# Kernel optimization log

Measured on AMD Instinct MI355X. Metric: run time of the kernel, lower is better.

## Reference

```python
import jax, jax.numpy as jnp
import numpy as np

EPS = 10.0
MAX_ITER = 50
THRESH = 1e-05
N, M, D = 8192, 8192, 32


def setup_inputs() -> dict:
    key = jax.random.key(0)
    k1, k2, k3, k4 = jax.random.split(key, 4)
    x = jax.random.normal(k1, (N, D), dtype=jnp.float32)
    y = jax.random.normal(k2, (M, D), dtype=jnp.float32)
    p = jax.random.uniform(k3, (N,), dtype=jnp.float32)
    q = jax.random.uniform(k4, (M,), dtype=jnp.float32)
    p = p / jnp.sum(p)  # marginals must be probability vectors
    q = q / jnp.sum(q)
    return {"x": x, "y": y, "p": p, "q": q}


def _cost_matrix_l2(x, y):
    # ||x_i - y_j||^2 via the expansion, avoiding the [N, M, D] intermediate
    x2 = jnp.sum(x * x, axis=-1)  # [N]
    y2 = jnp.sum(y * y, axis=-1)  # [M]
    C = x2[:, None] + y2[None, :] - 2.0 * (x @ y.T)  # [N, M]
    return jnp.maximum(C, 0.0)


def reference(x, y, p, q):
    C = _cost_matrix_l2(x, y)          # [N, M]
    K = jnp.exp(-C / EPS)              # [N, M]

    def step(carry, _):
        a, b, done = carry
        a_new = p / (K @ b)            # [N]
        b_new = q / (K.T @ a_new)      # [M]
        err = jnp.linalg.norm(b_new - b)
        # emulate the early break: freeze (a, b) once err < thresh was hit
        a_out = jnp.where(done, a, a_new)
        b_out = jnp.where(done, b, b_new)
        done = jnp.logical_or(done, err < THRESH)
        return (a_out, b_out, done), None

    init = (jnp.zeros_like(p), jnp.ones_like(q), jnp.array(False))
    (a, b, _), _ = jax.lax.scan(step, init, None, length=MAX_ITER)

    T = a[:, None] * K * b[None, :]    # diag(a) @ K @ diag(b)
    w_cost = jnp.sum(T * C)
    return w_cost, T
```

## Files before the change

kernel.cpp:

```cpp
#include <hip/hip_runtime.h>
#include <hip/hip_fp16.h>


#define NN 8192
#define DDIM 32
#define EPSF 10.0f
#define LOG2E 1.44269504088896340736f
#define LN2F 0.69314718055994530942f
#define KLOG2 8.0f
#define THRESH2 1e-10f

#define OFF_KS   0ull
#define OFF_PART (67108864ull)
#define OFF_A    (OFF_PART + 8388608ull)
#define OFF_B    (OFF_A + 32768ull)
#define OFF_X2   (OFF_B + 32768ull)
#define OFF_Y2   (OFF_X2 + 32768ull)
#define OFF_ERR  (OFF_Y2 + 32768ull)
#define WS_NEEDED (OFF_ERR + 4096ull)

typedef float floatx2 __attribute__((ext_vector_type(2)));

#if __has_builtin(__builtin_amdgcn_cvt_pk_f32_fp8) && __has_builtin(__builtin_amdgcn_cvt_pk_fp8_f32)
#define HW_FP8 1
#else
#define HW_FP8 0
#include <hip/hip_fp8.h>
#endif

__device__ __forceinline__ void fp8x4_to_f32(unsigned int w, float* f) {
#if HW_FP8
    floatx2 lo = __builtin_amdgcn_cvt_pk_f32_fp8((int)w, false);
    floatx2 hi = __builtin_amdgcn_cvt_pk_f32_fp8((int)w, true);
    f[0] = lo.x; f[1] = lo.y; f[2] = hi.x; f[3] = hi.y;
#else
    for (int i = 0; i < 4; ++i) {
        __hip_fp8_e4m3 h; h.__x = (__hip_fp8_storage_t)((w >> (8 * i)) & 0xff);
        f[i] = (float)h;
    }
#endif
}

__device__ __forceinline__ unsigned char f32_to_fp8(float v) {
#if HW_FP8
    return (unsigned char)(__builtin_amdgcn_cvt_pk_fp8_f32(v, v, 0, false) & 0xff);
#else
    __hip_fp8_e4m3 h(v);
    return (unsigned char)h.__x;
#endif
}

__device__ __forceinline__ bool is_done(const float* __restrict__ errpart) {
    float e = 0.f;
    for (int k = 0; k < 256; ++k) e += errpart[k];
    return e < THRESH2;
}

__global__ __launch_bounds__(256) void k_init(const float* __restrict__ x,
                                              const float* __restrict__ y,
                                              float* __restrict__ x2,
                                              float* __restrict__ y2,
                                              float* __restrict__ b,
                                              float* __restrict__ errpart,
                                              float* __restrict__ out) {
    int t = blockIdx.x * 256 + threadIdx.x;
    const float4* x4 = (const float4*)(x + (size_t)t * DDIM);
    float s = 0.f;
#pragma unroll
    for (int k = 0; k < 8; ++k) { float4 v = x4[k]; s += v.x*v.x + v.y*v.y + v.z*v.z + v.w*v.w; }
    x2[t] = s;
    const float4* y4 = (const float4*)(y + (size_t)t * DDIM);
    s = 0.f;
#pragma unroll
    for (int k = 0; k < 8; ++k) { float4 v = y4[k]; s += v.x*v.x + v.y*v.y + v.z*v.z + v.w*v.w; }
    y2[t] = s;
    b[t] = 1.0f;
    if (t < 256) errpart[t] = 1e30f;
    if (t == 0) out[0] = 0.f;
}

__global__ __launch_bounds__(256) void k_build(const float* __restrict__ x,
                                               const float* __restrict__ y,
                                               const float* __restrict__ x2,
                                               const float* __restrict__ y2,
                                               unsigned char* __restrict__ Ks) {
    __shared__ float yT[DDIM][256];
    __shared__ float xT[DDIM][32];
    __shared__ __align__(16) unsigned char hb8[32][256];
    const int t = threadIdx.x;
    const int jb = blockIdx.x & 31;
    const int ib = blockIdx.x >> 5;
    const int colbase = jb * 256, rowbase = ib * 32;

    {
        const float4* yp = (const float4*)(y + (size_t)(colbase + t) * DDIM);
#pragma unroll
        for (int k = 0; k < 8; ++k) {
            float4 v = yp[k];
            yT[4*k+0][t] = v.x; yT[4*k+1][t] = v.y; yT[4*k+2][t] = v.z; yT[4*k+3][t] = v.w;
        }
    }
    {
        int r = t >> 3, ds = (t & 7) * 4;
        float4 v = *(const float4*)(x + (size_t)(rowbase + r) * DDIM + ds);
        xT[ds+0][r] = v.x; xT[ds+1][r] = v.y; xT[ds+2][r] = v.z; xT[ds+3][r] = v.w;
    }
    __syncthreads();

    float acc[32];
#pragma unroll
    for (int r = 0; r < 32; ++r) acc[r] = 0.f;
    for (int d = 0; d < DDIM; ++d) {
        float yv = yT[d][t];
#pragma unroll
        for (int r4 = 0; r4 < 8; ++r4) {
            float4 xv = *(const float4*)&xT[d][r4 * 4];
            acc[r4*4+0] = fmaf(xv.x, yv, acc[r4*4+0]);
            acc[r4*4+1] = fmaf(xv.y, yv, acc[r4*4+1]);
            acc[r4*4+2] = fmaf(xv.z, yv, acc[r4*4+2]);
            acc[r4*4+3] = fmaf(xv.w, yv, acc[r4*4+3]);
        }
    }
    const float y2c = y2[colbase + t];
#pragma unroll
    for (int r = 0; r < 32; ++r) {
        float Cv = fmaxf(x2[rowbase + r] + y2c - 2.f * acc[r], 0.f);
        float arg = KLOG2 - Cv * (LOG2E / EPSF);
        hb8[r][t] = f32_to_fp8(__builtin_amdgcn_exp2f(arg));
    }
    __syncthreads();
    {
        int row = t >> 3, off = (t & 7) * 32;
        uint4 v0 = *(const uint4*)&hb8[row][off];
        uint4 v1 = *(const uint4*)&hb8[row][off + 16];
        unsigned char* dst = Ks + (size_t)(rowbase + row) * NN + colbase + off;
        *(uint4*)dst = v0;
        *(uint4*)(dst + 16) = v1;
    }
}

__global__ __launch_bounds__(1024) void k_iter(const unsigned char* __restrict__ Ks,
                                               const float* __restrict__ bg,
                                               const float* __restrict__ p,
                                               float* __restrict__ a_out,
                                               float* __restrict__ part,
                                               const float* __restrict__ errpart) {
    if (is_done(errpart)) return;
    __shared__ float bsw[NN];
    __shared__ float arow[32];
    __shared__ float rowhalf[8][2];
    const int t = threadIdx.x;
    const int w = t >> 6, lane = t & 63;
    const int band = blockIdx.x * 32;

    {
        float4 g0 = ((const float4*)bg)[2 * t];
        float4 g1 = ((const float4*)bg)[2 * t + 1];
        float vals[8] = {g0.x, g0.y, g0.z, g0.w, g1.x, g1.y, g1.z, g1.w};
        int c0 = t * 8;
#pragma unroll
        for (int u = 0; u < 8; ++u) {
            int c = c0 + u;
            bsw[(c >> 10) * 1024 + ((c >> 2) & 3) * 256 + ((c >> 4) & 63) * 4 + (c & 3)] = vals[u];
        }
    }
    __syncthreads();

    float cacc[8] = {0.f, 0.f, 0.f, 0.f, 0.f, 0.f, 0.f, 0.f};
    const float4* b4 = (const float4*)bsw;

    for (int sub = 0; sub < 4; ++sub) {
        const int rl = w >> 1, half = w & 1;
        const int rglob = band + sub * 8 + rl;
        const uint4* kp = (const uint4*)(Ks + (size_t)rglob * NN + half * 4096);
        float rs = 0.f;
#pragma unroll
        for (int c = 0; c < 4; ++c) {
            uint4 kv = kp[c * 64 + lane];
            const unsigned int* kw = (const unsigned int*)&kv;
            const int kc = half * 4 + c;
#pragma unroll
            for (int j4 = 0; j4 < 4; ++j4) {
                float kf[4];
                fp8x4_to_f32(kw[j4], kf);
                float4 bv = b4[(kc * 4 + j4) * 64 + lane];
                rs = fmaf(kf[0], bv.x, rs);
                rs = fmaf(kf[1], bv.y, rs);
                rs = fmaf(kf[2], bv.z, rs);
                rs = fmaf(kf[3], bv.w, rs);
            }
        }
#pragma unroll
        for (int off = 32; off > 0; off >>= 1) rs += __shfl_down(rs, off, 64);
        if (lane == 0) rowhalf[rl][half] = rs;
        __syncthreads();
        if (t < 8) {
            int rg = band + sub * 8 + t;
            float av = p[rg] / (rowhalf[t][0] + rowhalf[t][1]);
            arow[sub * 8 + t] = av;
            a_out[rg] = av;
        }
        __syncthreads();
        const uint2* kp2 = (const uint2*)(Ks + (size_t)(band + sub * 8) * NN);
#pragma unroll
        for (int r8 = 0; r8 < 8; ++r8) {
            uint2 kv = kp2[r8 * (NN / 8) + t];
            float kf[8];
            fp8x4_to_f32(kv.x, kf);
            fp8x4_to_f32(kv.y, kf + 4);
            float av = arow[sub * 8 + r8];
#pragma unroll
            for (int j = 0; j < 8; ++j) cacc[j] = fmaf(kf[j], av, cacc[j]);
        }
    }
    float4* pp = (float4*)(part + (size_t)blockIdx.x * NN + t * 8);
    pp[0] = make_float4(cacc[0], cacc[1], cacc[2], cacc[3]);
    pp[1] = make_float4(cacc[4], cacc[5], cacc[6], cacc[7]);
}

__global__ __launch_bounds__(256) void k_div(const float* __restrict__ part,
                                             const float* __restrict__ q,
                                             float* __restrict__ b,
                                             float* __restrict__ errpart) {
    if (is_done(errpart)) return;
    const int t = threadIdx.x;
    const int c = t & 31, ibc = t >> 5;
    const int col = blockIdx.x * 32 + c;
    float s = 0.f;
#pragma unroll 4
    for (int i = 0; i < 32; ++i) s += part[(size_t)(ibc * 32 + i) * NN + col];
    __shared__ float red[8][32];
    __shared__ float esc[32];
    red[ibc][c] = s;
    __syncthreads();
    if (ibc == 0) {
        float sum = 0.f;
#pragma unroll
        for (int k = 0; k < 8; ++k) sum += red[k][c];
        float bn = q[col] / sum;
        float d = bn - b[col];
        b[col] = bn;
        esc[c] = d * d;
    }
    __syncthreads();
    if (t == 0) {
        float e = 0.f;
#pragma unroll
        for (int k = 0; k < 32; ++k) e += esc[k];
        errpart[blockIdx.x] = e;
    }
}

__global__ __launch_bounds__(256) void k_final(const unsigned char* __restrict__ Ks,
                                               const float* __restrict__ a,
                                               const float* __restrict__ b,
                                               float* __restrict__ out) {
    const int t = threadIdx.x;
    const int row = blockIdx.x;
    const float ai = a[row];
    const uint2* kp = (const uint2*)(Ks + (size_t)row * NN);
    float* Trow = out + 1 + (size_t)row * NN;
    float w = 0.f;
    const float c1 = EPSF * LN2F;
#pragma unroll
    for (int k = 0; k < 4; ++k) {
        const int col = k * 2048 + t * 8;
        uint2 kv = kp[k * 256 + t];
        float kf[8];
        fp8x4_to_f32(kv.x, kf);
        fp8x4_to_f32(kv.y, kf + 4);
        float4 b0 = *(const float4*)(b + col);
        float4 b1 = *(const float4*)(b + col + 4);
        float bv[8] = {b0.x, b0.y, b0.z, b0.w, b1.x, b1.y, b1.z, b1.w};
#pragma unroll
        for (int j = 0; j < 8; ++j) {
            float ks = kf[j];
            float Tv = ai * ks * bv[j];
            float Cv = c1 * (KLOG2 - __builtin_amdgcn_logf(fmaxf(ks, 1e-35f)));
            w = fmaf(Tv, Cv, w);
            Trow[col + j] = Tv;
        }
    }
#pragma unroll
    for (int off = 32; off > 0; off >>= 1) w += __shfl_down(w, off, 64);
    __shared__ float red[4];
    if ((t & 63) == 0) red[t >> 6] = w;
    __syncthreads();
    if (t == 0) atomicAdd(out, (red[0] + red[1]) + (red[2] + red[3]));
}

extern "C" void kernel_launch(void* const* d_in, const int* in_sizes, int n_in,
                              void* d_out, int out_size, void* d_ws, size_t ws_size,
                              hipStream_t stream) {
    const float* x = (const float*)d_in[0];
    const float* y = (const float*)d_in[1];
    const float* p = (const float*)d_in[2];
    const float* q = (const float*)d_in[3];
    float* out = (float*)d_out;
    if (ws_size < WS_NEEDED) return;
    char* ws = (char*)d_ws;
    unsigned char* Ks = (unsigned char*)(ws + OFF_KS);
    float* part = (float*)(ws + OFF_PART);
    float* a = (float*)(ws + OFF_A);
    float* b = (float*)(ws + OFF_B);
    float* x2 = (float*)(ws + OFF_X2);
    float* y2 = (float*)(ws + OFF_Y2);
    float* errpart = (float*)(ws + OFF_ERR);

    k_init<<<dim3(32), dim3(256), 0, stream>>>(x, y, x2, y2, b, errpart, out);
    k_build<<<dim3(8192), dim3(256), 0, stream>>>(x, y, x2, y2, Ks);
    for (int it = 0; it < 50; ++it) {
        k_iter<<<dim3(256), dim3(1024), 0, stream>>>(Ks, b, p, a, part, errpart);
        k_div<<<dim3(256), dim3(256), 0, stream>>>(part, q, b, errpart);
    }
    k_final<<<dim3(8192), dim3(256), 0, stream>>>(Ks, a, b, out);
}
```

Baseline: 2.076 ms.

## Prefetch next K rows and parallelize convergence check in Sinkhorn iteration kernels

```diff
diff --git a/kernel.cpp b/kernel.cpp
--- a/kernel.cpp
+++ b/kernel.cpp
@@ -48,12 +48,6 @@
     __hip_fp8_e4m3 h(v);
     return (unsigned char)h.__x;
 #endif
-}
-
-__device__ __forceinline__ bool is_done(const float* __restrict__ errpart) {
-    float e = 0.f;
-    for (int k = 0; k < 256; ++k) e += errpart[k];
-    return e < THRESH2;
 }
 
 __global__ __launch_bounds__(256) void k_init(const float* __restrict__ x,
@@ -139,23 +133,56 @@
     }
 }
 
+#define ROWFMA(KV, KC) { \
+    const unsigned int* kw_ = (const unsigned int*)&(KV); \
+    _Pragma("unroll") \
+    for (int j4 = 0; j4 < 4; ++j4) { \
+        float kf_[4]; \
+        fp8x4_to_f32(kw_[j4], kf_); \
+        float4 bv_ = b4[((KC) * 4 + j4) * 64 + lane]; \
+        rs = fmaf(kf_[0], bv_.x, rs); \
+        rs = fmaf(kf_[1], bv_.y, rs); \
+        rs = fmaf(kf_[2], bv_.z, rs); \
+        rs = fmaf(kf_[3], bv_.w, rs); \
+    } }
+
+#define COLFMA(KV, AV) { \
+    float kf_[8]; \
+    fp8x4_to_f32((KV).x, kf_); \
+    fp8x4_to_f32((KV).y, kf_ + 4); \
+    _Pragma("unroll") \
+    for (int j = 0; j < 8; ++j) cacc[j] = fmaf(kf_[j], (AV), cacc[j]); }
+
 __global__ __launch_bounds__(1024) void k_iter(const unsigned char* __restrict__ Ks,
                                                const float* __restrict__ bg,
                                                const float* __restrict__ p,
                                                float* __restrict__ a_out,
                                                float* __restrict__ part,
                                                const float* __restrict__ errpart) {
-    if (is_done(errpart)) return;
     __shared__ float bsw[NN];
-    __shared__ float arow[32];
-    __shared__ float rowhalf[8][2];
+    __shared__ float rowhalf[2][8][2];
+    __shared__ float dred[17];
     const int t = threadIdx.x;
     const int w = t >> 6, lane = t & 63;
     const int band = blockIdx.x * 32;
-
-    {
-        float4 g0 = ((const float4*)bg)[2 * t];
-        float4 g1 = ((const float4*)bg)[2 * t + 1];
+    const int rl = w >> 1, half = w & 1;
+
+    float4 g0 = ((const float4*)bg)[2 * t];
+    float4 g1 = ((const float4*)bg)[2 * t + 1];
+    float e = (t < 256) ? errpart[t] : 0.f;
+    const uint4* kp0 = (const uint4*)(Ks + (size_t)(band + rl) * NN + half * 4096);
+    uint4 ka0 = kp0[lane], ka1 = kp0[64 + lane], ka2 = kp0[128 + lane], ka3 = kp0[192 + lane];
+    __builtin_amdgcn_sched_barrier(0);
+
+#pragma unroll
+    for (int off = 32; off > 0; off >>= 1) e += __shfl_down(e, off, 64);
+    if (lane == 0) dred[w] = e;
+    __syncthreads();
+    if (t == 0) dred[16] = (dred[0] + dred[1]) + (dred[2] + dred[3]);
+    __syncthreads();
+    if (dred[16] < THRESH2) return;
+
+    {
         float vals[8] = {g0.x, g0.y, g0.z, g0.w, g1.x, g1.y, g1.z, g1.w};
         int c0 = t * 8;
 #pragma unroll
@@ -169,49 +196,55 @@
     float cacc[8] = {0.f, 0.f, 0.f, 0.f, 0.f, 0.f, 0.f, 0.f};
     const float4* b4 = (const float4*)bsw;
 
+#pragma unroll
     for (int sub = 0; sub < 4; ++sub) {
-        const int rl = w >> 1, half = w & 1;
-        const int rglob = band + sub * 8 + rl;
-        const uint4* kp = (const uint4*)(Ks + (size_t)rglob * NN + half * 4096);
+        const int sb = sub & 1;
+        const uint2* kp2 = (const uint2*)(Ks + (size_t)(band + sub * 8) * NN);
+        uint2 cv0 = kp2[0 * (NN / 8) + t], cv1 = kp2[1 * (NN / 8) + t],
+              cv2 = kp2[2 * (NN / 8) + t], cv3 = kp2[3 * (NN / 8) + t],
+              cv4 = kp2[4 * (NN / 8) + t], cv5 = kp2[5 * (NN / 8) + t],
+              cv6 = kp2[6 * (NN / 8) + t], cv7 = kp2[7 * (NN / 8) + t];
+        uint4 kb0 = {0,0,0,0}, kb1 = {0,0,0,0}, kb2 = {0,0,0,0}, kb3 = {0,0,0,0};
+        if (sub < 3) {
+            const uint4* kp = (const uint4*)(Ks + (size_t)(band + (sub + 1) * 8 + rl) * NN + half * 4096);
+            kb0 = kp[lane]; kb1 = kp[64 + lane]; kb2 = kp[128 + lane]; kb3 = kp[192 + lane];
+        }
+        __builtin_amdgcn_sched_barrier(0);
+
         float rs = 0.f;
-#pragma unroll
-        for (int c = 0; c < 4; ++c) {
-            uint4 kv = kp[c * 64 + lane];
-            const unsigned int* kw = (const unsigned int*)&kv;
-            const int kc = half * 4 + c;
-#pragma unroll
-            for (int j4 = 0; j4 < 4; ++j4) {
-                float kf[4];
-                fp8x4_to_f32(kw[j4], kf);
-                float4 bv = b4[(kc * 4 + j4) * 64 + lane];
-                rs = fmaf(kf[0], bv.x, rs);
-                rs = fmaf(kf[1], bv.y, rs);
-                rs = fmaf(kf[2], bv.z, rs);
-                rs = fmaf(kf[3], bv.w, rs);
-            }
-        }
+        ROWFMA(ka0, half * 4 + 0)
+        ROWFMA(ka1, half * 4 + 1)
+        ROWFMA(ka2, half * 4 + 2)
+        ROWFMA(ka3, half * 4 + 3)
 #pragma unroll
         for (int off = 32; off > 0; off >>= 1) rs += __shfl_down(rs, off, 64);
-        if (lane == 0) rowhalf[rl][half] = rs;
+        if (lane == 0) rowhalf[sb][rl][half] = rs;
         __syncthreads();
-        if (t < 8) {
-            int rg = band + sub * 8 + t;
-            float av = p[rg] / (rowhalf[t][0] + rowhalf[t][1]);
-            arow[sub * 8 + t] = av;
-            a_out[rg] = av;
-        }
-        __syncthreads();
-        const uint2* kp2 = (const uint2*)(Ks + (size_t)(band + sub * 8) * NN);
-#pragma unroll
-        for (int r8 = 0; r8 < 8; ++r8) {
-            uint2 kv = kp2[r8 * (NN / 8) + t];
-            float kf[8];
-            fp8x4_to_f32(kv.x, kf);
-            fp8x4_to_f32(kv.y, kf + 4);
-            float av = arow[sub * 8 + r8];
-#pragma unroll
-            for (int j = 0; j < 8; ++j) cacc[j] = fmaf(kf[j], av, cacc[j]);
-        }
+
+        const int rg = band + sub * 8;
+        float av0 = p[rg + 0] / (rowhalf[sb][0][0] + rowhalf[sb][0][1]);
+        float av1 = p[rg + 1] / (rowhalf[sb][1][0] + rowhalf[sb][1][1]);
+        float av2 = p[rg + 2] / (rowhalf[sb][2][0] + rowhalf[sb][2][1]);
+        float av3 = p[rg + 3] / (rowhalf[sb][3][0] + rowhalf[sb][3][1]);
+        float av4 = p[rg + 4] / (rowhalf[sb][4][0] + rowhalf[sb][4][1]);
+        float av5 = p[rg + 5] / (rowhalf[sb][5][0] + rowhalf[sb][5][1]);
+        float av6 = p[rg + 6] / (rowhalf[sb][6][0] + rowhalf[sb][6][1]);
+        float av7 = p[rg + 7] / (rowhalf[sb][7][0] + rowhalf[sb][7][1]);
+        if (t == 0) {
+            *(float4*)(a_out + rg)     = make_float4(av0, av1, av2, av3);
+            *(float4*)(a_out + rg + 4) = make_float4(av4, av5, av6, av7);
+        }
+
+        COLFMA(cv0, av0)
+        COLFMA(cv1, av1)
+        COLFMA(cv2, av2)
+        COLFMA(cv3, av3)
+        COLFMA(cv4, av4)
+        COLFMA(cv5, av5)
+        COLFMA(cv6, av6)
+        COLFMA(cv7, av7)
+
+        if (sub < 3) { ka0 = kb0; ka1 = kb1; ka2 = kb2; ka3 = kb3; }
     }
     float4* pp = (float4*)(part + (size_t)blockIdx.x * NN + t * 8);
     pp[0] = make_float4(cacc[0], cacc[1], cacc[2], cacc[3]);
@@ -222,15 +255,25 @@
                                              const float* __restrict__ q,
                                              float* __restrict__ b,
                                              float* __restrict__ errpart) {
-    if (is_done(errpart)) return;
     const int t = threadIdx.x;
+    __shared__ float red[8][32];
+    __shared__ float esc[32];
+    __shared__ float dsum[5];
+    {
+        float e = errpart[t];
+#pragma unroll
+        for (int off = 32; off > 0; off >>= 1) e += __shfl_down(e, off, 64);
+        if ((t & 63) == 0) dsum[t >> 6] = e;
+        __syncthreads();
+        if (t == 0) dsum[4] = (dsum[0] + dsum[1]) + (dsum[2] + dsum[3]);
+        __syncthreads();
+        if (dsum[4] < THRESH2) return;
+    }
     const int c = t & 31, ibc = t >> 5;
     const int col = blockIdx.x * 32 + c;
     float s = 0.f;
 #pragma unroll 4
     for (int i = 0; i < 32; ++i) s += part[(size_t)(ibc * 32 + i) * NN + col];
-    __shared__ float red[8][32];
-    __shared__ float esc[32];
     red[ibc][c] = s;
     __syncthreads();
     if (ibc == 0) {
```

New measurement: 1.755 ms. 15.5% less time.

## Load K band once into registers and reuse for row and column products

Applied to the files above, without the earlier changes.

```diff
diff --git a/kernel.cpp b/kernel.cpp
--- a/kernel.cpp
+++ b/kernel.cpp
@@ -50,18 +50,12 @@
 #endif
 }
 
-__device__ __forceinline__ bool is_done(const float* __restrict__ errpart) {
-    float e = 0.f;
-    for (int k = 0; k < 256; ++k) e += errpart[k];
-    return e < THRESH2;
-}
-
 __global__ __launch_bounds__(256) void k_init(const float* __restrict__ x,
                                               const float* __restrict__ y,
                                               float* __restrict__ x2,
                                               float* __restrict__ y2,
                                               float* __restrict__ b,
-                                              float* __restrict__ errpart,
+                                              float* __restrict__ err,
                                               float* __restrict__ out) {
     int t = blockIdx.x * 256 + threadIdx.x;
     const float4* x4 = (const float4*)(x + (size_t)t * DDIM);
@@ -75,7 +69,7 @@
     for (int k = 0; k < 8; ++k) { float4 v = y4[k]; s += v.x*v.x + v.y*v.y + v.z*v.z + v.w*v.w; }
     y2[t] = s;
     b[t] = 1.0f;
-    if (t < 256) errpart[t] = 1e30f;
+    if (t < 2) err[t] = 1e30f;
     if (t == 0) out[0] = 0.f;
 }
 
@@ -139,79 +133,117 @@
     }
 }
 
+__device__ __forceinline__ float rowdot8(uint2 kv, const float4 b0, const float4 b1) {
+    float kf[8];
+    fp8x4_to_f32(kv.x, kf);
+    fp8x4_to_f32(kv.y, kf + 4);
+    float r = kf[0] * b0.x;
+    r = fmaf(kf[1], b0.y, r); r = fmaf(kf[2], b0.z, r); r = fmaf(kf[3], b0.w, r);
+    r = fmaf(kf[4], b1.x, r); r = fmaf(kf[5], b1.y, r);
+    r = fmaf(kf[6], b1.z, r); r = fmaf(kf[7], b1.w, r);
+    return r;
+}
+
+__device__ __forceinline__ void colfma8(uint2 kv, float av, float* cacc) {
+    float kf[8];
+    fp8x4_to_f32(kv.x, kf);
+    fp8x4_to_f32(kv.y, kf + 4);
+#pragma unroll
+    for (int j = 0; j < 8; ++j) cacc[j] = fmaf(kf[j], av, cacc[j]);
+}
+
+__device__ __forceinline__ float wave_reduce_rows8(float s0, float s1, float s2, float s3,
+                                                   float s4, float s5, float s6, float s7,
+                                                   int lane) {
+    const bool q0 = lane & 1, q1 = lane & 2, q2 = lane & 4;
+    float e0 = q0 ? s1 : s0, o0 = q0 ? s0 : s1;
+    float e1 = q0 ? s3 : s2, o1 = q0 ? s2 : s3;
+    float e2 = q0 ? s5 : s4, o2 = q0 ? s4 : s5;
+    float e3 = q0 ? s7 : s6, o3 = q0 ? s6 : s7;
+    e0 += __shfl_xor(o0, 1, 64);
+    e1 += __shfl_xor(o1, 1, 64);
+    e2 += __shfl_xor(o2, 1, 64);
+    e3 += __shfl_xor(o3, 1, 64);
+    float f0 = q1 ? e1 : e0, g0 = q1 ? e0 : e1;
+    float f1 = q1 ? e3 : e2, g1 = q1 ? e2 : e3;
+    f0 += __shfl_xor(g0, 2, 64);
+    f1 += __shfl_xor(g1, 2, 64);
+    float h = q2 ? f1 : f0, i8 = q2 ? f0 : f1;
+    h += __shfl_xor(i8, 4, 64);
+    h += __shfl_xor(h, 8, 64);
+    h += __shfl_xor(h, 16, 64);
+    h += __shfl_xor(h, 32, 64);
+    return h;
+}
+
 __global__ __launch_bounds__(1024) void k_iter(const unsigned char* __restrict__ Ks,
                                                const float* __restrict__ bg,
                                                const float* __restrict__ p,
                                                float* __restrict__ a_out,
                                                float* __restrict__ part,
-                                               const float* __restrict__ errpart) {
-    if (is_done(errpart)) return;
-    __shared__ float bsw[NN];
-    __shared__ float arow[32];
-    __shared__ float rowhalf[8][2];
+                                               float* __restrict__ err, int it) {
     const int t = threadIdx.x;
+    if (blockIdx.x == 0 && t == 0) err[it & 1] = 0.f;
+    if (err[(it ^ 1) & 1] < THRESH2) return;
+
     const int w = t >> 6, lane = t & 63;
-    const int band = blockIdx.x * 32;
-
-    {
-        float4 g0 = ((const float4*)bg)[2 * t];
-        float4 g1 = ((const float4*)bg)[2 * t + 1];
-        float vals[8] = {g0.x, g0.y, g0.z, g0.w, g1.x, g1.y, g1.z, g1.w};
-        int c0 = t * 8;
-#pragma unroll
-        for (int u = 0; u < 8; ++u) {
-            int c = c0 + u;
-            bsw[(c >> 10) * 1024 + ((c >> 2) & 3) * 256 + ((c >> 4) & 63) * 4 + (c & 3)] = vals[u];
-        }
-    }
-    __syncthreads();
+    const int band = blockIdx.x << 5;
+
+    const float4 bv0 = ((const float4*)bg)[2 * t];
+    const float4 bv1 = ((const float4*)bg)[2 * t + 1];
+    float pv = 0.f;
+    if (w == 0 && lane < 32) pv = p[band + lane];
+
+    __shared__ float wred[2][16][8];
+    __shared__ float a8s[2][8];
+
+    const uint2* kp = (const uint2*)(Ks + (size_t)band * NN) + t;
+    uint2 c0 = kp[0 * 1024], c1 = kp[1 * 1024], c2 = kp[2 * 1024], c3 = kp[3 * 1024],
+          c4 = kp[4 * 1024], c5 = kp[5 * 1024], c6 = kp[6 * 1024], c7 = kp[7 * 1024];
 
     float cacc[8] = {0.f, 0.f, 0.f, 0.f, 0.f, 0.f, 0.f, 0.f};
-    const float4* b4 = (const float4*)bsw;
-
+
+#pragma unroll
     for (int sub = 0; sub < 4; ++sub) {
-        const int rl = w >> 1, half = w & 1;
-        const int rglob = band + sub * 8 + rl;
-        const uint4* kp = (const uint4*)(Ks + (size_t)rglob * NN + half * 4096);
-        float rs = 0.f;
-#pragma unroll
-        for (int c = 0; c < 4; ++c) {
-            uint4 kv = kp[c * 64 + lane];
-            const unsigned int* kw = (const unsigned int*)&kv;
-            const int kc = half * 4 + c;
-#pragma unroll
-            for (int j4 = 0; j4 < 4; ++j4) {
-                float kf[4];
-                fp8x4_to_f32(kw[j4], kf);
-                float4 bv = b4[(kc * 4 + j4) * 64 + lane];
-                rs = fmaf(kf[0], bv.x, rs);
-                rs = fmaf(kf[1], bv.y, rs);
-                rs = fmaf(kf[2], bv.z, rs);
-                rs = fmaf(kf[3], bv.w, rs);
+        const int sb = sub & 1;
+        uint2 n0 = c0, n1 = c1, n2 = c2, n3 = c3, n4 = c4, n5 = c5, n6 = c6, n7 = c7;
+        if (sub < 3) {
+            const uint2* kn = kp + (size_t)(sub + 1) * 8 * 1024;
+            n0 = kn[0 * 1024]; n1 = kn[1 * 1024]; n2 = kn[2 * 1024]; n3 = kn[3 * 1024];
+            n4 = kn[4 * 1024]; n5 = kn[5 * 1024]; n6 = kn[6 * 1024]; n7 = kn[7 * 1024];
+        }
+        __builtin_amdgcn_sched_barrier(0);
+
+        float s0 = rowdot8(c0, bv0, bv1), s1 = rowdot8(c1, bv0, bv1);
+        float s2 = rowdot8(c2, bv0, bv1), s3 = rowdot8(c3, bv0, bv1);
+        float s4 = rowdot8(c4, bv0, bv1), s5 = rowdot8(c5, bv0, bv1);
+        float s6 = rowdot8(c6, bv0, bv1), s7 = rowdot8(c7, bv0, bv1);
+        float h = wave_reduce_rows8(s0, s1, s2, s3, s4, s5, s6, s7, lane);
+        if (lane < 8) wred[sb][w][lane] = h;
+        __syncthreads();
+
+        if (w == 0) {
+            float v = wred[sb][lane >> 3][lane & 7] + wred[sb][8 + (lane >> 3)][lane & 7];
+            v += __shfl_xor(v, 8, 64);
+            v += __shfl_xor(v, 16, 64);
+            v += __shfl_xor(v, 32, 64);
+            float pw = __shfl(pv, sub * 8 + (lane & 7), 64);
+            if (lane < 8) {
+                float av = pw / v;
+                a8s[sb][lane] = av;
+                a_out[band + sub * 8 + lane] = av;
             }
         }
-#pragma unroll
-        for (int off = 32; off > 0; off >>= 1) rs += __shfl_down(rs, off, 64);
-        if (lane == 0) rowhalf[rl][half] = rs;
         __syncthreads();
-        if (t < 8) {
-            int rg = band + sub * 8 + t;
-            float av = p[rg] / (rowhalf[t][0] + rowhalf[t][1]);
-            arow[sub * 8 + t] = av;
-            a_out[rg] = av;
-        }
-        __syncthreads();
-        const uint2* kp2 = (const uint2*)(Ks + (size_t)(band + sub * 8) * NN);
-#pragma unroll
-        for (int r8 = 0; r8 < 8; ++r8) {
-            uint2 kv = kp2[r8 * (NN / 8) + t];
-            float kf[8];
-            fp8x4_to_f32(kv.x, kf);
-            fp8x4_to_f32(kv.y, kf + 4);
-            float av = arow[sub * 8 + r8];
-#pragma unroll
-            for (int j = 0; j < 8; ++j) cacc[j] = fmaf(kf[j], av, cacc[j]);
-        }
+
+        const float4 aA = *(const float4*)&a8s[sb][0];
+        const float4 aB = *(const float4*)&a8s[sb][4];
+        colfma8(c0, aA.x, cacc); colfma8(c1, aA.y, cacc);
+        colfma8(c2, aA.z, cacc); colfma8(c3, aA.w, cacc);
+        colfma8(c4, aB.x, cacc); colfma8(c5, aB.y, cacc);
+        colfma8(c6, aB.z, cacc); colfma8(c7, aB.w, cacc);
+
+        c0 = n0; c1 = n1; c2 = n2; c3 = n3; c4 = n4; c5 = n5; c6 = n6; c7 = n7;
     }
     float4* pp = (float4*)(part + (size_t)blockIdx.x * NN + t * 8);
     pp[0] = make_float4(cacc[0], cacc[1], cacc[2], cacc[3]);
@@ -221,8 +253,8 @@
 __global__ __launch_bounds__(256) void k_div(const float* __restrict__ part,
                                              const float* __restrict__ q,
                                              float* __restrict__ b,
-                                             float* __restrict__ errpart) {
-    if (is_done(errpart)) return;
+                                             float* __restrict__ err, int it) {
+    if (err[(it ^ 1) & 1] < THRESH2) return;
     const int t = threadIdx.x;
     const int c = t & 31, ibc = t >> 5;
     const int col = blockIdx.x * 32 + c;
@@ -247,7 +279,7 @@
         float e = 0.f;
 #pragma unroll
         for (int k = 0; k < 32; ++k) e += esc[k];
-        errpart[blockIdx.x] = e;
+        atomicAdd(&err[it & 1], e);
     }
 }
 
@@ -305,13 +337,13 @@
     float* b = (float*)(ws + OFF_B);
     float* x2 = (float*)(ws + OFF_X2);
     float* y2 = (float*)(ws + OFF_Y2);
-    float* errpart = (float*)(ws + OFF_ERR);
-
-    k_init<<<dim3(32), dim3(256), 0, stream>>>(x, y, x2, y2, b, errpart, out);
+    float* err = (float*)(ws + OFF_ERR);
+
+    k_init<<<dim3(32), dim3(256), 0, stream>>>(x, y, x2, y2, b, err, out);
     k_build<<<dim3(8192), dim3(256), 0, stream>>>(x, y, x2, y2, Ks);
     for (int it = 0; it < 50; ++it) {
-        k_iter<<<dim3(256), dim3(1024), 0, stream>>>(Ks, b, p, a, part, errpart);
-        k_div<<<dim3(256), dim3(256), 0, stream>>>(part, q, b, errpart);
+        k_iter<<<dim3(256), dim3(1024), 0, stream>>>(Ks, b, p, a, part, err, it);
+        k_div<<<dim3(256), dim3(256), 0, stream>>>(part, q, b, err, it);
     }
     k_final<<<dim3(8192), dim3(256), 0, stream>>>(Ks, a, b, out);
 }
```

Measured after the change: 3.755 ms. 80.9% more time.
